# Optimization experiments

Hardware: AMD Instinct MI355X
Metric: run time of the kernel (lower is better)

The kernel has to match this reference:

```python
import jax, jax.numpy as jnp
import numpy as np

N = 256        # number of nodes (= len(num_nodes_phases))
F = 16         # max_features = max(num_nodes_phases)
H = 2048       # hidden_dim
P = 16         # phases per node (uniform -> all q heads output P)
E = 32768      # directed edges


def setup_inputs() -> dict:
    key = jax.random.key(0)
    k1, k2, k3, k4 = jax.random.split(key, 4)
    x_list = jax.random.normal(k1, (N, F), dtype=jnp.float32)
    edge_index = jax.random.randint(k2, (2, E), 0, N, dtype=jnp.int64)
    # GCNConv weight/bias (PyG: x @ W then aggregate, bias added after)
    W = jax.random.normal(k3, (F, H), dtype=jnp.float32) * (1.0 / np.sqrt(F))
    b = jnp.zeros((H,), dtype=jnp.float32)
    # per-node q-value heads, stacked: Wq[n] is the n-th nn.Linear(H, P)
    Wq = jax.random.normal(k4, (N, H, P), dtype=jnp.float32) * (1.0 / np.sqrt(H))
    bq = jnp.zeros((N, P), dtype=jnp.float32)
    return {"x_list": x_list, "edge_index": edge_index, "W": W, "b": b, "Wq": Wq, "bq": bq}


def reference(x_list, edge_index, W, b, Wq, bq):
    n = x_list.shape[0]
    # GCNConv: add self-loops, symmetric degree normalization
    loops = jnp.arange(n, dtype=edge_index.dtype)
    src = jnp.concatenate([edge_index[0], loops])
    dst = jnp.concatenate([edge_index[1], loops])
    deg = jax.ops.segment_sum(jnp.ones_like(dst, dtype=x_list.dtype), dst, num_segments=n)
    dinv = jnp.where(deg > 0, jax.lax.rsqrt(deg), 0.0).astype(x_list.dtype)
    norm = dinv[src] * dinv[dst]                      # [E+N]
    h = x_list @ W                                    # [N, H]
    msg = h[src] * norm[:, None]                      # [E+N, H] (dominant traffic)
    out = jax.ops.segment_sum(msg, dst, num_segments=n) + b  # [N, H]
    # per-node-type linear heads (batched over nodes)
    q = jnp.einsum('nh,nhp->np', out, Wq) + bq        # [N, P]
    return q
```

## Files before the change

kernel.cpp:

```cpp
#include <hip/hip_runtime.h>

#define N_NODES 256
#define F_DIM   16
#define H_DIM   2048
#define P_DIM   16
#define E_EDGES 32768


__global__ __launch_bounds__(256) void k_cnt(const int* __restrict__ ei,
                                             float* __restrict__ cntT) {
    int e = blockIdx.x * 256 + threadIdx.x;
    int s = ei[e];
    int d = ei[E_EDGES + e];
    atomicAdd(&cntT[s * N_NODES + d], 1.0f);
}

__global__ __launch_bounds__(256) void k_node(
    const float* __restrict__ cntT, const float* __restrict__ x,
    const float* __restrict__ W, const float* __restrict__ b,
    const float* __restrict__ Wq, const float* __restrict__ bq,
    float* __restrict__ qout)
{
    __shared__ float part[4][256];
    __shared__ float dinv[N_NODES];
    __shared__ float xlT[F_DIM][N_NODES];
    __shared__ float g[F_DIM];
    __shared__ float red[4][P_DIM];

    const int n = blockIdx.x;
    const int t = threadIdx.x;
    const int w = t >> 6, l = t & 63;

    if (t < F_DIM) g[t] = 0.0f;

    {
        const float4* x4 = (const float4*)(x + t * F_DIM);
        float4 a0 = x4[0], a1 = x4[1], a2 = x4[2], a3 = x4[3];
        xlT[0][t]  = a0.x; xlT[1][t]  = a0.y; xlT[2][t]  = a0.z; xlT[3][t]  = a0.w;
        xlT[4][t]  = a1.x; xlT[5][t]  = a1.y; xlT[6][t]  = a1.z; xlT[7][t]  = a1.w;
        xlT[8][t]  = a2.x; xlT[9][t]  = a2.y; xlT[10][t] = a2.z; xlT[11][t] = a2.w;
        xlT[12][t] = a3.x; xlT[13][t] = a3.y; xlT[14][t] = a3.z; xlT[15][t] = a3.w;
    }

    {
        const float4* cT4 = (const float4*)cntT;
        float4 sum = {0.f, 0.f, 0.f, 0.f};
        int s0 = w * 64;
#pragma unroll 16
        for (int s = s0; s < s0 + 64; ++s) {
            float4 v = cT4[s * 64 + l];
            sum.x += v.x; sum.y += v.y; sum.z += v.z; sum.w += v.w;
        }
        *(float4*)&part[w][4 * l] = sum;
    }
    __syncthreads();

    if (t < 64) {
        float4 a0 = *(float4*)&part[0][4 * t];
        float4 a1 = *(float4*)&part[1][4 * t];
        float4 a2 = *(float4*)&part[2][4 * t];
        float4 a3 = *(float4*)&part[3][4 * t];
        dinv[4 * t + 0] = rsqrtf(a0.x + a1.x + a2.x + a3.x + 1.0f);
        dinv[4 * t + 1] = rsqrtf(a0.y + a1.y + a2.y + a3.y + 1.0f);
        dinv[4 * t + 2] = rsqrtf(a0.z + a1.z + a2.z + a3.z + 1.0f);
        dinv[4 * t + 3] = rsqrtf(a0.w + a1.w + a2.w + a3.w + 1.0f);
    }
    __syncthreads();

    {
        float a = cntT[t * N_NODES + n] + (t == n ? 1.0f : 0.0f);
        a *= dinv[t];
        if (a != 0.0f) {
#pragma unroll
            for (int f = 0; f < F_DIM; ++f)
                atomicAdd(&g[f], a * xlT[f][t]);
        }
    }
    __syncthreads();

    float dn = dinv[n];
    float gr[F_DIM];
#pragma unroll
    for (int f = 0; f < F_DIM; ++f) gr[f] = g[f] * dn;

    float o[8];
#pragma unroll
    for (int i = 0; i < 8; ++i) {
        int hh = t + 256 * i;
        float v = b[hh];
#pragma unroll
        for (int f = 0; f < F_DIM; ++f)
            v += gr[f] * W[f * H_DIM + hh];
        o[i] = v;
    }

    float acc[16];
#pragma unroll
    for (int p = 0; p < 16; ++p) acc[p] = 0.0f;
    const float4* Wqn = (const float4*)(Wq + (size_t)n * H_DIM * P_DIM);
#pragma unroll
    for (int i = 0; i < 8; ++i) {
        int hh = t + 256 * i;
        float ov = o[i];
        float4 u0 = Wqn[hh * 4 + 0];
        float4 u1 = Wqn[hh * 4 + 1];
        float4 u2 = Wqn[hh * 4 + 2];
        float4 u3 = Wqn[hh * 4 + 3];
        acc[0]  += ov * u0.x; acc[1]  += ov * u0.y; acc[2]  += ov * u0.z; acc[3]  += ov * u0.w;
        acc[4]  += ov * u1.x; acc[5]  += ov * u1.y; acc[6]  += ov * u1.z; acc[7]  += ov * u1.w;
        acc[8]  += ov * u2.x; acc[9]  += ov * u2.y; acc[10] += ov * u2.z; acc[11] += ov * u2.w;
        acc[12] += ov * u3.x; acc[13] += ov * u3.y; acc[14] += ov * u3.z; acc[15] += ov * u3.w;
    }

#pragma unroll
    for (int p = 0; p < 16; ++p)
#pragma unroll
        for (int off = 32; off > 0; off >>= 1)
            acc[p] += __shfl_down(acc[p], off, 64);

    if (l == 0) {
#pragma unroll
        for (int p = 0; p < 16; ++p) red[w][p] = acc[p];
    }
    __syncthreads();
    if (t < P_DIM) {
        float s = red[0][t] + red[1][t] + red[2][t] + red[3][t] +
                  bq[n * P_DIM + t];
        qout[n * P_DIM + t] = s;
    }
}

extern "C" void kernel_launch(void* const* d_in, const int* in_sizes, int n_in,
                              void* d_out, int out_size, void* d_ws, size_t ws_size,
                              hipStream_t stream) {
    const float* x  = (const float*)d_in[0];
    const int*   ei = (const int*)d_in[1];
    const float* W  = (const float*)d_in[2];
    const float* b  = (const float*)d_in[3];
    const float* Wq = (const float*)d_in[4];
    const float* bq = (const float*)d_in[5];
    float* qout = (float*)d_out;

    float* cntT = (float*)d_ws;

    hipMemsetAsync(cntT, 0, N_NODES * N_NODES * sizeof(float), stream);
    k_cnt <<<128, 256, 0, stream>>>(ei, cntT);
    k_node<<<N_NODES, 256, 0, stream>>>(cntT, x, W, b, Wq, bq, qout);
}
```

Measured before the change: 111.3 us.

## Precompute degrees with atomics, transpose count matrix, prefetch Wq into registers

The count kernel now stores counts in destination-major order and also accumulates per-node degrees with atomics. This removes the per-block full 256x256 column-sum pass each node block used to rebuild dinv. The node kernel uses 512 threads, issues all Wq loads for its node up front into registers to overlap them with the aggregation, and swaps shared-memory atomics for wavefront shuffle reductions. The cost is extra atomic contention on the degree array and higher register pressure from holding 16 float4 values per thread.

```diff
diff --git a/kernel.cpp b/kernel.cpp
--- a/kernel.cpp
+++ b/kernel.cpp
@@ -5,88 +5,82 @@
 #define H_DIM   2048
 #define P_DIM   16
 #define E_EDGES 32768
+#define BLK     512
 
 
 __global__ __launch_bounds__(256) void k_cnt(const int* __restrict__ ei,
-                                             float* __restrict__ cntT) {
+                                             float* __restrict__ cnt,
+                                             float* __restrict__ deg) {
     int e = blockIdx.x * 256 + threadIdx.x;
     int s = ei[e];
     int d = ei[E_EDGES + e];
-    atomicAdd(&cntT[s * N_NODES + d], 1.0f);
+    atomicAdd(&cnt[d * N_NODES + s], 1.0f);
+    atomicAdd(&deg[d], 1.0f);
 }
 
-__global__ __launch_bounds__(256) void k_node(
-    const float* __restrict__ cntT, const float* __restrict__ x,
-    const float* __restrict__ W, const float* __restrict__ b,
-    const float* __restrict__ Wq, const float* __restrict__ bq,
-    float* __restrict__ qout)
+__global__ __launch_bounds__(BLK) void k_node(
+    const float* __restrict__ cnt, const float* __restrict__ deg,
+    const float* __restrict__ x,   const float* __restrict__ W,
+    const float* __restrict__ b,   const float* __restrict__ Wq,
+    const float* __restrict__ bq,  float* __restrict__ qout)
 {
-    __shared__ float part[4][256];
-    __shared__ float dinv[N_NODES];
-    __shared__ float xlT[F_DIM][N_NODES];
-    __shared__ float g[F_DIM];
-    __shared__ float red[4][P_DIM];
+    __shared__ float gw[4][F_DIM];
+    __shared__ float gfin[F_DIM];
+    __shared__ float red[BLK / 64][P_DIM];
 
     const int n = blockIdx.x;
     const int t = threadIdx.x;
     const int w = t >> 6, l = t & 63;
 
-    if (t < F_DIM) g[t] = 0.0f;
+    const float4* Wqn = (const float4*)(Wq + (size_t)n * (H_DIM * P_DIM));
+    float4 u00, u01, u02, u03, u10, u11, u12, u13;
+    float4 u20, u21, u22, u23, u30, u31, u32, u33;
+    {
+        int h0 = (t          ) * 4;
+        int h1 = (t +     BLK) * 4;
+        int h2 = (t + 2 * BLK) * 4;
+        int h3 = (t + 3 * BLK) * 4;
+        u00 = Wqn[h0 + 0]; u01 = Wqn[h0 + 1]; u02 = Wqn[h0 + 2]; u03 = Wqn[h0 + 3];
+        u10 = Wqn[h1 + 0]; u11 = Wqn[h1 + 1]; u12 = Wqn[h1 + 2]; u13 = Wqn[h1 + 3];
+        u20 = Wqn[h2 + 0]; u21 = Wqn[h2 + 1]; u22 = Wqn[h2 + 2]; u23 = Wqn[h2 + 3];
+        u30 = Wqn[h3 + 0]; u31 = Wqn[h3 + 1]; u32 = Wqn[h3 + 2]; u33 = Wqn[h3 + 3];
+    }
 
-    {
+    float dn = rsqrtf(deg[n] + 1.0f);
+
+    if (t < N_NODES) {
+        float dt = rsqrtf(deg[t] + 1.0f);
+        float a  = (cnt[n * N_NODES + t] + (t == n ? 1.0f : 0.0f)) * dt;
         const float4* x4 = (const float4*)(x + t * F_DIM);
         float4 a0 = x4[0], a1 = x4[1], a2 = x4[2], a3 = x4[3];
-        xlT[0][t]  = a0.x; xlT[1][t]  = a0.y; xlT[2][t]  = a0.z; xlT[3][t]  = a0.w;
-        xlT[4][t]  = a1.x; xlT[5][t]  = a1.y; xlT[6][t]  = a1.z; xlT[7][t]  = a1.w;
-        xlT[8][t]  = a2.x; xlT[9][t]  = a2.y; xlT[10][t] = a2.z; xlT[11][t] = a2.w;
-        xlT[12][t] = a3.x; xlT[13][t] = a3.y; xlT[14][t] = a3.z; xlT[15][t] = a3.w;
-    }
-
-    {
-        const float4* cT4 = (const float4*)cntT;
-        float4 sum = {0.f, 0.f, 0.f, 0.f};
-        int s0 = w * 64;
-#pragma unroll 16
-        for (int s = s0; s < s0 + 64; ++s) {
-            float4 v = cT4[s * 64 + l];
-            sum.x += v.x; sum.y += v.y; sum.z += v.z; sum.w += v.w;
-        }
-        *(float4*)&part[w][4 * l] = sum;
-    }
-    __syncthreads();
-
-    if (t < 64) {
-        float4 a0 = *(float4*)&part[0][4 * t];
-        float4 a1 = *(float4*)&part[1][4 * t];
-        float4 a2 = *(float4*)&part[2][4 * t];
-        float4 a3 = *(float4*)&part[3][4 * t];
-        dinv[4 * t + 0] = rsqrtf(a0.x + a1.x + a2.x + a3.x + 1.0f);
-        dinv[4 * t + 1] = rsqrtf(a0.y + a1.y + a2.y + a3.y + 1.0f);
-        dinv[4 * t + 2] = rsqrtf(a0.z + a1.z + a2.z + a3.z + 1.0f);
-        dinv[4 * t + 3] = rsqrtf(a0.w + a1.w + a2.w + a3.w + 1.0f);
-    }
-    __syncthreads();
-
-    {
-        float a = cntT[t * N_NODES + n] + (t == n ? 1.0f : 0.0f);
-        a *= dinv[t];
-        if (a != 0.0f) {
+        float val[F_DIM];
+        val[0]  = a * a0.x; val[1]  = a * a0.y; val[2]  = a * a0.z; val[3]  = a * a0.w;
+        val[4]  = a * a1.x; val[5]  = a * a1.y; val[6]  = a * a1.z; val[7]  = a * a1.w;
+        val[8]  = a * a2.x; val[9]  = a * a2.y; val[10] = a * a2.z; val[11] = a * a2.w;
+        val[12] = a * a3.x; val[13] = a * a3.y; val[14] = a * a3.z; val[15] = a * a3.w;
 #pragma unroll
-            for (int f = 0; f < F_DIM; ++f)
-                atomicAdd(&g[f], a * xlT[f][t]);
+        for (int f = 0; f < F_DIM; ++f)
+#pragma unroll
+            for (int off = 32; off > 0; off >>= 1)
+                val[f] += __shfl_xor(val[f], off, 64);
+        if (l == 0) {
+#pragma unroll
+            for (int f = 0; f < F_DIM; ++f) gw[w][f] = val[f];
         }
     }
     __syncthreads();
+    if (t < F_DIM)
+        gfin[t] = gw[0][t] + gw[1][t] + gw[2][t] + gw[3][t];
+    __syncthreads();
 
-    float dn = dinv[n];
     float gr[F_DIM];
 #pragma unroll
-    for (int f = 0; f < F_DIM; ++f) gr[f] = g[f] * dn;
+    for (int f = 0; f < F_DIM; ++f) gr[f] = gfin[f] * dn;
 
-    float o[8];
+    float o[4];
 #pragma unroll
-    for (int i = 0; i < 8; ++i) {
-        int hh = t + 256 * i;
+    for (int i = 0; i < 4; ++i) {
+        int hh = t + BLK * i;
         float v = b[hh];
 #pragma unroll
         for (int f = 0; f < F_DIM; ++f)
@@ -97,20 +91,18 @@
     float acc[16];
 #pragma unroll
     for (int p = 0; p < 16; ++p) acc[p] = 0.0f;
-    const float4* Wqn = (const float4*)(Wq + (size_t)n * H_DIM * P_DIM);
-#pragma unroll
-    for (int i = 0; i < 8; ++i) {
-        int hh = t + 256 * i;
-        float ov = o[i];
-        float4 u0 = Wqn[hh * 4 + 0];
-        float4 u1 = Wqn[hh * 4 + 1];
-        float4 u2 = Wqn[hh * 4 + 2];
-        float4 u3 = Wqn[hh * 4 + 3];
-        acc[0]  += ov * u0.x; acc[1]  += ov * u0.y; acc[2]  += ov * u0.z; acc[3]  += ov * u0.w;
-        acc[4]  += ov * u1.x; acc[5]  += ov * u1.y; acc[6]  += ov * u1.z; acc[7]  += ov * u1.w;
-        acc[8]  += ov * u2.x; acc[9]  += ov * u2.y; acc[10] += ov * u2.z; acc[11] += ov * u2.w;
-        acc[12] += ov * u3.x; acc[13] += ov * u3.y; acc[14] += ov * u3.z; acc[15] += ov * u3.w;
-    }
+
+#define ACC4(OV, U0, U1, U2, U3) { float ov = (OV);                            \
+    acc[0]  += ov * U0.x; acc[1]  += ov * U0.y; acc[2]  += ov * U0.z; acc[3]  += ov * U0.w; \
+    acc[4]  += ov * U1.x; acc[5]  += ov * U1.y; acc[6]  += ov * U1.z; acc[7]  += ov * U1.w; \
+    acc[8]  += ov * U2.x; acc[9]  += ov * U2.y; acc[10] += ov * U2.z; acc[11] += ov * U2.w; \
+    acc[12] += ov * U3.x; acc[13] += ov * U3.y; acc[14] += ov * U3.z; acc[15] += ov * U3.w; }
+
+    ACC4(o[0], u00, u01, u02, u03)
+    ACC4(o[1], u10, u11, u12, u13)
+    ACC4(o[2], u20, u21, u22, u23)
+    ACC4(o[3], u30, u31, u32, u33)
+#undef ACC4
 
 #pragma unroll
     for (int p = 0; p < 16; ++p)
@@ -124,8 +116,9 @@
     }
     __syncthreads();
     if (t < P_DIM) {
-        float s = red[0][t] + red[1][t] + red[2][t] + red[3][t] +
-                  bq[n * P_DIM + t];
+        float s = bq[n * P_DIM + t];
+#pragma unroll
+        for (int ww = 0; ww < BLK / 64; ++ww) s += red[ww][t];
         qout[n * P_DIM + t] = s;
     }
 }
@@ -141,9 +134,10 @@
     const float* bq = (const float*)d_in[5];
     float* qout = (float*)d_out;
 
-    float* cntT = (float*)d_ws;
+    float* cnt = (float*)d_ws;
+    float* deg = cnt + N_NODES * N_NODES;
 
-    hipMemsetAsync(cntT, 0, N_NODES * N_NODES * sizeof(float), stream);
-    k_cnt <<<128, 256, 0, stream>>>(ei, cntT);
-    k_node<<<N_NODES, 256, 0, stream>>>(cntT, x, W, b, Wq, bq, qout);
+    hipMemsetAsync(d_ws, 0, (N_NODES * N_NODES + N_NODES) * sizeof(float), stream);
+    k_cnt <<<E_EDGES / 256, 256, 0, stream>>>(ei, cnt, deg);
+    k_node<<<N_NODES, BLK, 0, stream>>>(cnt, deg, x, W, b, Wq, bq, qout);
 }
```

Result: no change. 110.0 us (-1.2%).
